# Kernel optimization log

Hardware: AMD Instinct MI355X
Metric: run time of the kernel (lower is better)

The kernel has to match this reference:

```python
import jax, jax.numpy as jnp
import numpy as np

NUM_HEADS = 16

def setup_inputs() -> dict:
    key = jax.random.key(0)
    ks = jax.random.split(key, 11)
    B, S, D, H = 2, 2048, 1024, 1024
    s = lambda k, shape, scale=1.0: (jax.random.normal(k, shape, dtype=jnp.float32) * scale)
    return {
        "KEY": s(ks[0], (B, S, D)),
        "VALUE": s(ks[1], (B, S, D)),
        "QUERY": s(ks[2], (B, S, D)),
        "Wk_w": s(ks[3], (H, D), 0.02),
        "Wk_b": s(ks[4], (H,), 0.02),
        "Wq_w": s(ks[5], (H, D), 0.02),
        "Wq_b": s(ks[6], (H,), 0.02),
        "Wv_w": s(ks[7], (H, D), 0.02),
        "Wv_b": s(ks[8], (H,), 0.02),
        "Wo_w": s(ks[9], (H, H), 0.02),
        "Wo_b": s(ks[10], (H,), 0.02),
    }


def _split_heads(x, num_heads):
    # torch: reshape (B, S, dh, nh) then permute(0,3,1,2) -> (B, nh, S, dh)
    B, S, H = x.shape
    dh = H // num_heads
    return x.reshape(B, S, dh, num_heads).transpose(0, 3, 1, 2)


def reference(KEY, VALUE, QUERY, Wk_w, Wk_b, Wq_w, Wq_b, Wv_w, Wv_b, Wo_w, Wo_b):
    nh = NUM_HEADS
    k = _split_heads(KEY @ Wk_w.T + Wk_b, nh)      # [B, nh, Sk, dh]
    q = _split_heads(QUERY @ Wq_w.T + Wq_b, nh)    # [B, nh, Sq, dh]
    v = _split_heads(VALUE @ Wv_w.T + Wv_b, nh)    # [B, nh, Sv, dh]
    dh = q.shape[-1]
    score = jnp.einsum('bhij,bhkj->bhik', k, q) / jnp.sqrt(jnp.asarray(dh, k.dtype))  # [B,nh,Sk,Sq]
    # NOTE: faithful to the source — softmax over dim=1 (the HEAD axis)
    attn = jax.nn.softmax(score, axis=1)
    out = jnp.einsum('bhik,bhij->bhjk', attn, v)   # [B, nh, dh, Sq]
    B = out.shape[0]
    # permute(0,2,1,3) -> [B, dh, nh, Sq]; reshape -> [B, dh*nh, Sq]; transpose -> [B, Sq, H]
    out = out.transpose(0, 2, 1, 3).reshape(B, -1, out.shape[-1]).transpose(0, 2, 1)
    res = out @ Wo_w.T + Wo_b                      # dropout is identity in eval mode
    return res
```

## Files before the change

### kernel.cpp

```cpp
#include <hip/hip_runtime.h>
#include <hip/hip_bf16.h>

typedef __attribute__((ext_vector_type(8))) short s8v;
typedef __attribute__((ext_vector_type(4))) short s4v;
typedef __attribute__((ext_vector_type(4))) float f4v;

#define MFMA32(A,B,C) __builtin_amdgcn_mfma_f32_16x16x32_bf16(A,B,C,0,0,0)
#define MFMA16(A,B,C) __builtin_amdgcn_mfma_f32_16x16x16bf16_1k(A,B,C,0,0,0)

typedef __attribute__((address_space(1))) const void* gas1;
typedef __attribute__((address_space(3))) void* las3;
#define GLDS16(g,l) __builtin_amdgcn_global_load_lds((gas1)(const void*)(g),(las3)(void*)(l),16,0,0)

__device__ __forceinline__ unsigned short f2bf(float f){
  unsigned int u = __float_as_uint(f);
  u += 0x7FFFu + ((u>>16)&1u);
  return (unsigned short)(u>>16);
}
__device__ __forceinline__ float bf2f(unsigned short s){
  return __uint_as_float(((unsigned int)s)<<16);
}
__device__ __forceinline__ s4v pack4(f4v v){
  float2 lo; lo.x=v[0]; lo.y=v[1];
  float2 hi; hi.x=v[2]; hi.y=v[3];
  __hip_bfloat162 a = __float22bfloat162_rn(lo);
  __hip_bfloat162 b = __float22bfloat162_rn(hi);
  union{ s4v s; unsigned int u[2]; } r;
  __builtin_memcpy(&r.u[0], &a, 4);
  __builtin_memcpy(&r.u[1], &b, 4);
  return r.s;
}

#define EXPC 0.18033688011112042f

#define BARRIER() do{                                        \
  asm volatile("s_waitcnt lgkmcnt(0)" ::: "memory");         \
  __builtin_amdgcn_s_barrier();                              \
  asm volatile("" ::: "memory");                             \
}while(0)
#define VBARRIER() do{                                       \
  asm volatile("s_waitcnt vmcnt(0) lgkmcnt(0)" ::: "memory");\
  __builtin_amdgcn_s_barrier();                              \
  asm volatile("" ::: "memory");                             \
}while(0)

__global__ __launch_bounds__(256) void conv_in(
    const float* __restrict__ KEY, const float* __restrict__ QUERY, const float* __restrict__ VALUE,
    const float* __restrict__ Wk, const float* __restrict__ Wq, const float* __restrict__ Wv,
    unsigned short* __restrict__ kb, unsigned short* __restrict__ qb,
    unsigned short* __restrict__ vb, unsigned short* __restrict__ wkb,
    unsigned short* __restrict__ wqb, unsigned short* __restrict__ wvb)
{
  const int z = blockIdx.y;
  const size_t n = (z<3)? (size_t)4194304 : (size_t)1048576;
  size_t idx = ((size_t)blockIdx.x*256 + threadIdx.x)*8;
  if(idx >= n) return;
  const float* s = (z==0)?KEY:(z==1)?QUERY:(z==2)?VALUE:(z==3)?Wk:(z==4)?Wq:Wv;
  unsigned short* d = (z==0)?kb:(z==1)?qb:(z==2)?vb:(z==3)?wkb:(z==4)?wqb:wvb;
  float4 a = *(const float4*)&s[idx];
  float4 b = *(const float4*)&s[idx+4];
  union{ s8v v; s4v h[2]; } r;
  r.h[0]=pack4((f4v){a.x,a.y,a.z,a.w});
  r.h[1]=pack4((f4v){b.x,b.y,b.z,b.w});
  *(s8v*)&d[idx]=r.v;
}

__global__ __launch_bounds__(256) void pack_wo(const float* __restrict__ wo,
                                              unsigned short* __restrict__ wop){
  __shared__ unsigned short tile[4][1024];
  const int o0 = blockIdx.x*4;
  const int t = threadIdx.x;
  const int r = t>>6, u = t&63;
  #pragma unroll
  for(int e4=0;e4<4;e4++){
    float4 v = *(const float4*)&wo[(size_t)(o0+r)*1024 + u*16 + e4*4];
    tile[r][(e4*4+0)*64 + u] = f2bf(v.x);
    tile[r][(e4*4+1)*64 + u] = f2bf(v.y);
    tile[r][(e4*4+2)*64 + u] = f2bf(v.z);
    tile[r][(e4*4+3)*64 + u] = f2bf(v.w);
  }
  __syncthreads();
  const unsigned short* flat = &tile[0][0];
  *(s8v*)&wop[(size_t)o0*1024 + t*16]     = *(const s8v*)&flat[t*16];
  *(s8v*)&wop[(size_t)o0*1024 + t*16 + 8] = *(const s8v*)&flat[t*16 + 8];
}

__global__ __launch_bounds__(256) void proj_gemm(
    const unsigned short* __restrict__ kbp, const unsigned short* __restrict__ qbp,
    const unsigned short* __restrict__ vbp,
    const unsigned short* __restrict__ wkb, const unsigned short* __restrict__ wqb,
    const unsigned short* __restrict__ wvb,
    const float* __restrict__ bk, const float* __restrict__ bq, const float* __restrict__ bv,
    unsigned short* __restrict__ kh, unsigned short* __restrict__ qh,
    unsigned short* __restrict__ vt)
{
  __shared__ short As[128*64];
  __shared__ short Bs[128*64];
  const int t = threadIdx.x;
  const int z = blockIdx.z;
  const unsigned short* A; const unsigned short* W; const float* bias;
  if(z==0){A=kbp; W=wkb; bias=bk;}
  else if(z==1){A=qbp; W=wqb; bias=bq;}
  else {A=vbp; W=wvb; bias=bv;}
  const int m0 = blockIdx.x*128, n0 = blockIdx.y*128;
  const int l = t&63, w = t>>6;
  const int wm = (w>>1)*64, wn = (w&1)*64;
  const int row16 = l&15, quad = l>>4;
  f4v acc[4][4];
  #pragma unroll
  for(int i=0;i<4;i++)
    #pragma unroll
    for(int j=0;j<4;j++) acc[i][j] = (f4v){0.f,0.f,0.f,0.f};

  const int sr=t>>3, sc=(t&7)*8;
  for(int k0=0;k0<1024;k0+=64){
    #pragma unroll
    for(int p=0;p<4;p++){
      GLDS16(&A[(size_t)(m0+p*32+sr)*1024 + k0 + sc], &As[(p*32+sr)*64 + sc]);
      GLDS16(&W[(size_t)(n0+p*32+sr)*1024 + k0 + sc], &Bs[(p*32+sr)*64 + sc]);
    }
    __syncthreads();
    #pragma unroll
    for(int kk=0; kk<64; kk+=32){
      s8v af[4], bf[4];
      #pragma unroll
      for(int mt=0;mt<4;mt++) af[mt] = *(const s8v*)&As[(wm+mt*16+row16)*64 + kk + quad*8];
      #pragma unroll
      for(int nt=0;nt<4;nt++) bf[nt] = *(const s8v*)&Bs[(wn+nt*16+row16)*64 + kk + quad*8];
      #pragma unroll
      for(int mt=0;mt<4;mt++)
        #pragma unroll
        for(int nt=0;nt<4;nt++)
          acc[mt][nt] = MFMA32(af[mt], bf[nt], acc[mt][nt]);
    }
    __syncthreads();
  }

  const int jb = (n0+wn)>>4;
  const float bv0 = bias[n0+wn+ 0+row16];
  const float bv1 = bias[n0+wn+16+row16];
  const float bv2 = bias[n0+wn+32+row16];
  const float bv3 = bias[n0+wn+48+row16];
  if(z==2){
    #pragma unroll
    for(int mt=0;mt<4;mt++){
      const int m = m0+wm+mt*16;
      const int bb=m>>11, ss=m&2047, it=ss>>4;
      const size_t base = ((size_t)(bb*16+row16)*128 + it)*1024;
      #pragma unroll
      for(int nt=0;nt<4;nt++){
        const int jj = jb+nt;
        const int jp = jj>>5, r16j = jj&15, half = (jj>>4)&1;
        const int slot = (jp*16 + r16j)*4 + quad;
        const float bn = (nt==0)?bv0:(nt==1)?bv1:(nt==2)?bv2:bv3;
        f4v vals = {acc[mt][nt][0]+bn, acc[mt][nt][1]+bn,
                    acc[mt][nt][2]+bn, acc[mt][nt][3]+bn};
        *(s4v*)&vt[base + slot*8 + half*4] = pack4(vals);
      }
    }
  } else {
    unsigned short* dst = (z==0)? kh : qh;
    #pragma unroll
    for(int mt=0;mt<4;mt++){
      #pragma unroll
      for(int r=0;r<4;r++){
        const int m = m0+wm+mt*16+quad*4+r;
        const int bb=m>>11, ss=m&2047;
        f4v vals = {acc[mt][0][r]+bv0, acc[mt][1][r]+bv1,
                    acc[mt][2][r]+bv2, acc[mt][3][r]+bv3};
        *(s4v*)&dst[((size_t)(bb*16+row16)*2048 + ss)*64 + jb] = pack4(vals);
      }
    }
  }
}

__global__ __launch_bounds__(512) void fused_attn(
    const unsigned short* __restrict__ kh, const unsigned short* __restrict__ qh,
    const unsigned short* __restrict__ vt, unsigned short* __restrict__ opart)
{
  __shared__ unsigned short Ks[2][16384];
  __shared__ unsigned short Vs[2][16384];
  __shared__ f4v dpart[2][4][64];

  const int t=threadIdx.x, l=t&63, w=t>>6;
  const int qg=w>>2, hg=w&3;
  const int row16=l&15, quad=l>>4;
  const int bid=blockIdx.x;
  const int combo=bid&7, qb=bid>>3;
  const int ih=combo&3, b=combo>>2;
  const int q0=qb*32+qg*16, h0=hg*4;
  const int ibase=ih*512;

  s8v qf[4][2];
  #pragma unroll
  for(int hh=0;hh<4;hh++){
    const unsigned short* qp=&qh[(size_t)((b*16+h0+hh)*2048 + q0+row16)*64];
    qf[hh][0]=*(const s8v*)&qp[quad*8];
    qf[hh][1]=*(const s8v*)&qp[32+quad*8];
  }

  const unsigned short* kgs[4];
  const unsigned short* vgs[4];
  #pragma unroll
  for(int p=0;p<4;p++){
    const int v = p*512 + t;
    const int rr = v>>3, sl = (v&7)^(rr&7);
    const int h = rr>>4, i = rr&15;
    kgs[p] = &kh[((size_t)(b*16+h)*2048 + ibase + i)*64 + sl*8];
    const int hv = v>>7, slv = v&127;
    vgs[p] = &vt[((size_t)(b*16+hv)*128 + ih*32)*1024 + slv*8];
  }

  f4v o[4][4];
  #pragma unroll
  for(int i=0;i<4;i++)
    #pragma unroll
    for(int j=0;j<4;j++) o[i][j]=(f4v){0.f,0.f,0.f,0.f};

  #pragma unroll
  for(int p=0;p<4;p++) GLDS16(kgs[p], &Ks[0][(p*512+t)*8]);
  #pragma unroll
  for(int p=0;p<4;p++) GLDS16(vgs[p], &Vs[0][(p*512+t)*8]);
  VBARRIER();

  const int sw0=(quad^(row16&7))<<3, sw1=((quad+4)^(row16&7))<<3;

  #pragma unroll 1
  for(int it=0; it<32; ++it){
    const int cur=it&1, nxt=cur^1;
    const int offn=((it+1)&31)*1024;
    #pragma unroll
    for(int p=0;p<4;p++) GLDS16(kgs[p]+offn, &Ks[nxt][(p*512+t)*8]);
    #pragma unroll
    for(int p=0;p<4;p++) GLDS16(vgs[p]+offn, &Vs[nxt][(p*512+t)*8]);
    f4v e0[4];
    #pragma unroll
    for(int hh=0;hh<4;hh++){
      const unsigned short* kp=&Ks[cur][((h0+hh)*16+row16)*64];
      f4v S={0.f,0.f,0.f,0.f};
      S=MFMA32(*(const s8v*)&kp[sw0], qf[hh][0], S);
      S=MFMA32(*(const s8v*)&kp[sw1], qf[hh][1], S);
      #pragma unroll
      for(int r=0;r<4;r++) e0[hh][r]=__builtin_amdgcn_exp2f(S[r]*EXPC);
    }
    f4v d0=(e0[0]+e0[1])+(e0[2]+e0[3]);
    dpart[qg][hg][l]=d0;
    BARRIER();
    f4v s0=(dpart[qg][0][l]+dpart[qg][1][l])+(dpart[qg][2][l]+dpart[qg][3][l]);
    f4v r0;
    #pragma unroll
    for(int r=0;r<4;r++) r0[r]=__builtin_amdgcn_rcpf(s0[r]);
    s4v p0[4];
    #pragma unroll
    for(int hh=0;hh<4;hh++) p0[hh]=pack4(e0[hh]*r0);
    #pragma unroll
    for(int hh=0;hh<4;hh++){
      #pragma unroll
      for(int jp=0;jp<2;jp++){
        s8v vv=*(const s8v*)&Vs[cur][(h0+hh)*1024 + ((jp*16+row16)*4+quad)*8];
        s4v v0={vv[0],vv[1],vv[2],vv[3]};
        s4v v1={vv[4],vv[5],vv[6],vv[7]};
        o[hh][jp*2]  =MFMA16(v0, p0[hh], o[hh][jp*2]);
        o[hh][jp*2+1]=MFMA16(v1, p0[hh], o[hh][jp*2+1]);
      }
    }
    VBARRIER();
  }

  #pragma unroll
  for(int hh=0;hh<4;hh++)
    #pragma unroll
    for(int jt=0;jt<4;jt++)
      *(s4v*)&opart[(size_t)((ih*2+b)*2048 + q0+row16)*1024 + (h0+hh)*64 + jt*16 + quad*4]
        = pack4(o[hh][jt]);
}

__global__ __launch_bounds__(256) void reduce_o(
    const unsigned short* __restrict__ op, unsigned short* __restrict__ out2)
{
  size_t e = ((size_t)blockIdx.x*256 + threadIdx.x)*8;
  s8v a = *(const s8v*)&op[e];
  s8v b = *(const s8v*)&op[(size_t)4194304 + e];
  s8v c = *(const s8v*)&op[(size_t)2*4194304 + e];
  s8v d = *(const s8v*)&op[(size_t)3*4194304 + e];
  f4v lo, hi;
  #pragma unroll
  for(int i=0;i<4;i++)
    lo[i] = (bf2f((unsigned short)a[i])+bf2f((unsigned short)b[i]))
          + (bf2f((unsigned short)c[i])+bf2f((unsigned short)d[i]));
  #pragma unroll
  for(int i=0;i<4;i++)
    hi[i] = (bf2f((unsigned short)a[i+4])+bf2f((unsigned short)b[i+4]))
          + (bf2f((unsigned short)c[i+4])+bf2f((unsigned short)d[i+4]));
  *(s4v*)&out2[e]   = pack4(lo);
  *(s4v*)&out2[e+4] = pack4(hi);
}

__global__ __launch_bounds__(256) void out_gemm(
    const unsigned short* __restrict__ A, const unsigned short* __restrict__ Bm,
    const float* __restrict__ bias, float* __restrict__ out)
{
  __shared__ short As[128*64];
  __shared__ short Bs[128*64];
  const int t=threadIdx.x, l=t&63, w=t>>6;
  const int row16=l&15, quad=l>>4;
  const int m0=blockIdx.x*128, n0=blockIdx.y*128;
  const int wm=(w>>1)*64, wn=(w&1)*64;
  f4v acc[4][4];
  #pragma unroll
  for(int i=0;i<4;i++)
    #pragma unroll
    for(int j=0;j<4;j++) acc[i][j] = (f4v){0.f,0.f,0.f,0.f};

  const int sr=t>>3, sc=(t&7)*8;
  for(int k0=0;k0<1024;k0+=64){
    #pragma unroll
    for(int p=0;p<4;p++){
      GLDS16(&A [(size_t)(m0+p*32+sr)*1024 + k0 + sc], &As[(p*32+sr)*64 + sc]);
      GLDS16(&Bm[(size_t)(n0+p*32+sr)*1024 + k0 + sc], &Bs[(p*32+sr)*64 + sc]);
    }
    __syncthreads();
    #pragma unroll
    for(int kk=0; kk<64; kk+=32){
      s8v af[4], bf[4];
      #pragma unroll
      for(int mt=0;mt<4;mt++) af[mt] = *(const s8v*)&As[(wm+mt*16+row16)*64 + kk + quad*8];
      #pragma unroll
      for(int nt=0;nt<4;nt++) bf[nt] = *(const s8v*)&Bs[(wn+nt*16+row16)*64 + kk + quad*8];
      #pragma unroll
      for(int mt=0;mt<4;mt++)
        #pragma unroll
        for(int nt=0;nt<4;nt++)
          acc[mt][nt] = MFMA32(af[mt], bf[nt], acc[mt][nt]);
    }
    __syncthreads();
  }
  #pragma unroll
  for(int nt=0;nt<4;nt++){
    const int n = n0+wn+nt*16+row16;
    const float bias_n = bias[n];
    #pragma unroll
    for(int mt=0;mt<4;mt++)
      #pragma unroll
      for(int r=0;r<4;r++){
        const int m = m0+wm+mt*16+quad*4+r;
        out[(size_t)m*1024 + n] = acc[mt][nt][r] + bias_n;
      }
  }
}

extern "C" void kernel_launch(void* const* d_in, const int* in_sizes, int n_in,
                              void* d_out, int out_size, void* d_ws, size_t ws_size,
                              hipStream_t stream)
{
  const float* KEY   = (const float*)d_in[0];
  const float* VALUE = (const float*)d_in[1];
  const float* QUERY = (const float*)d_in[2];
  const float* Wk = (const float*)d_in[3];
  const float* bk = (const float*)d_in[4];
  const float* Wq = (const float*)d_in[5];
  const float* bq = (const float*)d_in[6];
  const float* Wv = (const float*)d_in[7];
  const float* bv = (const float*)d_in[8];
  const float* Wo = (const float*)d_in[9];
  const float* bo = (const float*)d_in[10];

  char* ws = (char*)d_ws;
  unsigned short* kb   = (unsigned short*)(ws);
  unsigned short* qb   = (unsigned short*)(ws +  8388608);
  unsigned short* vb   = (unsigned short*)(ws + 16777216);
  unsigned short* wkb  = (unsigned short*)(ws + 25165824);
  unsigned short* wqb  = (unsigned short*)(ws + 27262976);
  unsigned short* wvb  = (unsigned short*)(ws + 29360128);
  unsigned short* kh   = (unsigned short*)(ws + 33554432);
  unsigned short* qh   = (unsigned short*)(ws + 41943040);
  unsigned short* vt   = (unsigned short*)(ws + 50331648);
  unsigned short* opart= (unsigned short*)(ws);
  unsigned short* wop  = (unsigned short*)(ws + 33554432);
  unsigned short* out2 = (unsigned short*)(ws + 35651584);

  conv_in   <<<dim3(2048,6), dim3(256), 0, stream>>>(KEY,QUERY,VALUE,Wk,Wq,Wv,kb,qb,vb,wkb,wqb,wvb);
  proj_gemm <<<dim3(32,8,3), dim3(256), 0, stream>>>(kb,qb,vb,wkb,wqb,wvb,bk,bq,bv,kh,qh,vt);
  fused_attn<<<dim3(512),    dim3(512), 0, stream>>>(kh,qh,vt,opart);
  pack_wo   <<<dim3(256),    dim3(256), 0, stream>>>(Wo,wop);
  reduce_o  <<<dim3(2048),   dim3(256), 0, stream>>>(opart,out2);
  out_gemm  <<<dim3(32,8),   dim3(256), 0, stream>>>(out2,wop,bo,(float*)d_out);
}
```

Measured before the change: 316.3 us.

## Single-buffer K/V LDS tiles with staggered loads and new V layout

Replaces the double-buffered K and V shared-memory tiles with single buffers, halving LDS use. K for the next iteration is loaded after the score phase's barrier, and V is loaded at the start of each iteration. The V projection output is re-laid out as contiguous 16-element rows and read with a new XOR swizzle, and the per-thread global pointers are computed from one base plus fixed strides. The smaller LDS footprint may allow more blocks per CU, but the loads now overlap less with compute, which adds exposed latency inside the loop.

New measurement: 320.2 us. About the same (+1.2%).

```diff
diff --git a/kernel.cpp b/kernel.cpp
--- a/kernel.cpp
+++ b/kernel.cpp
@@ -146,16 +146,13 @@
     for(int mt=0;mt<4;mt++){
       const int m = m0+wm+mt*16;
       const int bb=m>>11, ss=m&2047, it=ss>>4;
-      const size_t base = ((size_t)(bb*16+row16)*128 + it)*1024;
+      const size_t base = (((size_t)(bb*16+row16))*128 + it)*64;
       #pragma unroll
       for(int nt=0;nt<4;nt++){
-        const int jj = jb+nt;
-        const int jp = jj>>5, r16j = jj&15, half = (jj>>4)&1;
-        const int slot = (jp*16 + r16j)*4 + quad;
         const float bn = (nt==0)?bv0:(nt==1)?bv1:(nt==2)?bv2:bv3;
         f4v vals = {acc[mt][nt][0]+bn, acc[mt][nt][1]+bn,
                     acc[mt][nt][2]+bn, acc[mt][nt][3]+bn};
-        *(s4v*)&vt[base + slot*8 + half*4] = pack4(vals);
+        *(s4v*)&vt[(base + jb+nt)*16 + quad*4] = pack4(vals);
       }
     }
   } else {
@@ -178,8 +175,8 @@
     const unsigned short* __restrict__ kh, const unsigned short* __restrict__ qh,
     const unsigned short* __restrict__ vt, unsigned short* __restrict__ opart)
 {
-  __shared__ unsigned short Ks[2][16384];
-  __shared__ unsigned short Vs[2][16384];
+  __shared__ unsigned short Ks[16384];
+  __shared__ unsigned short Vs[16384];
   __shared__ f4v dpart[2][4][64];
 
   const int t=threadIdx.x, l=t&63, w=t>>6;
@@ -199,17 +196,12 @@
     qf[hh][1]=*(const s8v*)&qp[32+quad*8];
   }
 
-  const unsigned short* kgs[4];
-  const unsigned short* vgs[4];
-  #pragma unroll
-  for(int p=0;p<4;p++){
-    const int v = p*512 + t;
-    const int rr = v>>3, sl = (v&7)^(rr&7);
-    const int h = rr>>4, i = rr&15;
-    kgs[p] = &kh[((size_t)(b*16+h)*2048 + ibase + i)*64 + sl*8];
-    const int hv = v>>7, slv = v&127;
-    vgs[p] = &vt[((size_t)(b*16+hv)*128 + ih*32)*1024 + slv*8];
-  }
+  const int slk = (t&7)^((t>>3)&7);
+  const unsigned short* kg0 =
+      &kh[((size_t)(b*16 + (t>>7))*2048 + ibase + ((t>>3)&15))*64 + slk*8];
+  const int lv16 = (t&1)^((t>>3)&1);
+  const unsigned short* vg0 =
+      &vt[((size_t)(b*16 + (t>>7))*128 + ih*32)*1024 + ((t>>1)&63)*16 + lv16*8];
 
   f4v o[4][4];
   #pragma unroll
@@ -218,25 +210,25 @@
     for(int j=0;j<4;j++) o[i][j]=(f4v){0.f,0.f,0.f,0.f};
 
   #pragma unroll
-  for(int p=0;p<4;p++) GLDS16(kgs[p], &Ks[0][(p*512+t)*8]);
-  #pragma unroll
-  for(int p=0;p<4;p++) GLDS16(vgs[p], &Vs[0][(p*512+t)*8]);
+  for(int p=0;p<4;p++) GLDS16(kg0 + (size_t)p*524288, &Ks[(p*512+t)*8]);
+  #pragma unroll
+  for(int p=0;p<4;p++) GLDS16(vg0 + (size_t)p*524288, &Vs[(p*512+t)*8]);
   VBARRIER();
 
   const int sw0=(quad^(row16&7))<<3, sw1=((quad+4)^(row16&7))<<3;
+  const int vro=(((quad>>1)^((row16>>2)&1))<<3) + ((quad&1)<<2);
 
   #pragma unroll 1
   for(int it=0; it<32; ++it){
-    const int cur=it&1, nxt=cur^1;
-    const int offn=((it+1)&31)*1024;
-    #pragma unroll
-    for(int p=0;p<4;p++) GLDS16(kgs[p]+offn, &Ks[nxt][(p*512+t)*8]);
-    #pragma unroll
-    for(int p=0;p<4;p++) GLDS16(vgs[p]+offn, &Vs[nxt][(p*512+t)*8]);
+    if(it){
+      const int offv = it*1024;
+      #pragma unroll
+      for(int p=0;p<4;p++) GLDS16(vg0 + offv + (size_t)p*524288, &Vs[(p*512+t)*8]);
+    }
     f4v e0[4];
     #pragma unroll
     for(int hh=0;hh<4;hh++){
-      const unsigned short* kp=&Ks[cur][((h0+hh)*16+row16)*64];
+      const unsigned short* kp=&Ks[((h0+hh)*16+row16)*64];
       f4v S={0.f,0.f,0.f,0.f};
       S=MFMA32(*(const s8v*)&kp[sw0], qf[hh][0], S);
       S=MFMA32(*(const s8v*)&kp[sw1], qf[hh][1], S);
@@ -245,7 +237,10 @@
     }
     f4v d0=(e0[0]+e0[1])+(e0[2]+e0[3]);
     dpart[qg][hg][l]=d0;
-    BARRIER();
+    VBARRIER();
+    const int offk = ((it+1)&31)*1024;
+    #pragma unroll
+    for(int p=0;p<4;p++) GLDS16(kg0 + offk + (size_t)p*524288, &Ks[(p*512+t)*8]);
     f4v s0=(dpart[qg][0][l]+dpart[qg][1][l])+(dpart[qg][2][l]+dpart[qg][3][l]);
     f4v r0;
     #pragma unroll
@@ -256,12 +251,10 @@
     #pragma unroll
     for(int hh=0;hh<4;hh++){
       #pragma unroll
-      for(int jp=0;jp<2;jp++){
-        s8v vv=*(const s8v*)&Vs[cur][(h0+hh)*1024 + ((jp*16+row16)*4+quad)*8];
-        s4v v0={vv[0],vv[1],vv[2],vv[3]};
-        s4v v1={vv[4],vv[5],vv[6],vv[7]};
-        o[hh][jp*2]  =MFMA16(v0, p0[hh], o[hh][jp*2]);
-        o[hh][jp*2+1]=MFMA16(v1, p0[hh], o[hh][jp*2+1]);
+      for(int jt=0;jt<4;jt++){
+        const int vrow=(h0+hh)*64+jt*16+row16;
+        s4v v0=*(const s4v*)&Vs[vrow*16 + vro];
+        o[hh][jt]=MFMA16(v0, p0[hh], o[hh][jt]);
       }
     }
     VBARRIER();
```
